# Optimization experiments

Measured on AMD Instinct MI355X. Metric: run time of the kernel, lower is better.

Reference implementation:

```python
import jax, jax.numpy as jnp
import numpy as np

D_MODEL = 1024
HIDDEN = 2816
N_EXPERTS = 8
N_ACTIVE = 2
THRESH = 1.0  # snntorch Leaky default threshold; single-step spike = (input > 1.0)


def setup_inputs() -> dict:
    key = jax.random.key(0)
    ks = jax.random.split(key, 10)
    s = 0.02
    return {
        "x": jax.random.normal(ks[0], (2, 1024, D_MODEL), jnp.float32),
        "Wg": jax.random.normal(ks[1], (D_MODEL, N_EXPERTS), jnp.float32) * s,
        "bg": jnp.zeros((N_EXPERTS,), jnp.float32),
        "W_gate": jax.random.normal(ks[2], (N_EXPERTS, D_MODEL, HIDDEN), jnp.float32) * s,
        "b_gate": jnp.zeros((N_EXPERTS, HIDDEN), jnp.float32),
        "W_up": jax.random.normal(ks[3], (N_EXPERTS, D_MODEL, HIDDEN), jnp.float32) * s,
        "b_up": jnp.zeros((N_EXPERTS, HIDDEN), jnp.float32),
        "W_down": jax.random.normal(ks[4], (N_EXPERTS, HIDDEN, D_MODEL), jnp.float32) * s,
        "b_down": jnp.zeros((N_EXPERTS, D_MODEL), jnp.float32),
    }


def reference(x, Wg, bg, W_gate, b_gate, W_up, b_up, W_down, b_down):
    B, S, D = x.shape
    xf = x.reshape(-1, D)  # [T, D]
    # spiking gate: single-step Leaky => spike = heaviside(logits - 1.0)
    gate_logits = xf @ Wg + bg  # [T, E]
    spike_out = (gate_logits > THRESH).astype(x.dtype)
    top_v, top_idx = jax.lax.top_k(spike_out, N_ACTIVE)  # [T, K]
    top_w = jax.nn.softmax(top_v, axis=-1)  # [T, K]
    # combine weights per expert: sum_k onehot(idx_k) * w_k  -> [T, E]
    combine = jnp.sum(jax.nn.one_hot(top_idx, N_EXPERTS, dtype=x.dtype) * top_w[..., None], axis=1)
    # per-expert SpikingSwiGLU: spike(gate_proj(x)) * up_proj(x) -> down_proj
    g = jnp.einsum("td,edh->teh", xf, W_gate) + b_gate  # [T, E, H]
    u = jnp.einsum("td,edh->teh", xf, W_up) + b_up
    h = (g > THRESH).astype(x.dtype) * u
    y = jnp.einsum("teh,ehd->ted", h, W_down) + b_down  # [T, E, D]
    out = jnp.einsum("ted,te->td", y, combine)
    return out.reshape(B, S, D)
```

## Files before the change

kernel.cpp:

```cpp
#include <hip/hip_runtime.h>


#define D_MODEL 1024
#define HID     2816
#define NEXP    8
#define NTOK    2048
#define NPAIR   4096
#define TM      128
#define FLAGCAP  65536
#define KC      384
#define BAND    3e-4f
#define INNER   2e-5
#define NBA     22
#define NBB     8
#define AMAX    128
#define BMAX    48

typedef short s8v __attribute__((ext_vector_type(8)));
typedef float f4v __attribute__((ext_vector_type(4)));

__device__ __forceinline__ unsigned short f2bf(float f) {
  unsigned u = __float_as_uint(f);
  u += 0x7FFFu + ((u >> 16) & 1u);
  return (unsigned short)(u >> 16);
}
__device__ __forceinline__ float bf2f(unsigned short s) {
  return __uint_as_float(((unsigned)s) << 16);
}

__device__ __forceinline__ void gld16(const unsigned short* g, unsigned short* l) {
  __builtin_amdgcn_global_load_lds(
      (const __attribute__((address_space(1))) void*)g,
      (__attribute__((address_space(3))) void*)l, 16, 0, 0);
}

__device__ __forceinline__ bool np_spike(const float* __restrict__ xr,
                                         const float* __restrict__ wcol,
                                         size_t stride, float bias) {
  float g = 0.0f;
  for (int p0 = 0; p0 < D_MODEL; p0 += KC) {
    const int pe = min(p0 + KC, D_MODEL);
    float s = 0.0f;
    for (int d = p0; d < pe; ++d)
      s = fmaf(xr[d], wcol[(size_t)d * stride], s);
    g += s;
  }
  g += bias;
  return g > 1.0f;
}

__global__ void k_convx(const float* __restrict__ x, unsigned short* __restrict__ xh,
                        unsigned short* __restrict__ xl) {
  const int i = blockIdx.x * 256 + threadIdx.x;
  const float4 v = ((const float4*)x)[i];
  ushort4 h, l;
  h.x = f2bf(v.x); l.x = f2bf(v.x - bf2f(h.x));
  h.y = f2bf(v.y); l.y = f2bf(v.y - bf2f(h.y));
  h.z = f2bf(v.z); l.z = f2bf(v.z - bf2f(h.z));
  h.w = f2bf(v.w); l.w = f2bf(v.w - bf2f(h.w));
  ((ushort4*)xh)[i] = h;
  ((ushort4*)xl)[i] = l;
}

__global__ void k_convw(const float* __restrict__ in, unsigned short* __restrict__ hi,
                        unsigned short* __restrict__ lo, int R, int C) {
  const int e = blockIdx.y;
  const int ntx = C >> 6;
  const int tx = blockIdx.x % ntx;
  const int ty = blockIdx.x / ntx;
  const float* src = in + (size_t)e * R * C;
  const size_t obase = (size_t)e * R * C;
  __shared__ float t[64][65];
  const int tid = threadIdx.x;
#pragma unroll
  for (int it = 0; it < 4; ++it) {
    const int r = it * 16 + (tid >> 4);
    const float4 v = *(const float4*)(src + (size_t)(ty * 64 + r) * C + tx * 64 + (tid & 15) * 4);
    t[r][(tid & 15) * 4 + 0] = v.x;
    t[r][(tid & 15) * 4 + 1] = v.y;
    t[r][(tid & 15) * 4 + 2] = v.z;
    t[r][(tid & 15) * 4 + 3] = v.w;
  }
  __syncthreads();
#pragma unroll
  for (int it = 0; it < 2; ++it) {
    const int c = it * 32 + (tid >> 3);
    const int d0 = (tid & 7) * 8;
    s8v vh, vl;
#pragma unroll
    for (int i = 0; i < 8; ++i) {
      const float f = t[d0 + i][c];
      const unsigned short h = f2bf(f);
      vh[i] = (short)h;
      vl[i] = (short)f2bf(f - bf2f(h));
    }
    const size_t o = obase + (size_t)(tx * 64 + c) * R + ty * 64 + d0;
    *(s8v*)(hi + o) = vh;
    if (lo) *(s8v*)(lo + o) = vl;
  }
}

__global__ void k_router(const float* __restrict__ x, const float* __restrict__ Wg,
                         const float* __restrict__ bg, int* __restrict__ top_e,
                         float* __restrict__ top_w) {
  const int t = (blockIdx.x * blockDim.x + threadIdx.x) >> 6;
  const int lane = threadIdx.x & 63;
  if (t >= NTOK) return;
  const float* xr = x + (size_t)t * D_MODEL;
  double acc[NEXP];
#pragma unroll
  for (int e = 0; e < NEXP; ++e) acc[e] = 0.0;
#pragma unroll
  for (int i = 0; i < D_MODEL / 64; ++i) {
    const int d = lane + 64 * i;
    const double xv = (double)xr[d];
    const float4 w0 = *(const float4*)(Wg + d * NEXP);
    const float4 w1 = *(const float4*)(Wg + d * NEXP + 4);
    acc[0] = fma(xv, (double)w0.x, acc[0]);
    acc[1] = fma(xv, (double)w0.y, acc[1]);
    acc[2] = fma(xv, (double)w0.z, acc[2]);
    acc[3] = fma(xv, (double)w0.w, acc[3]);
    acc[4] = fma(xv, (double)w1.x, acc[4]);
    acc[5] = fma(xv, (double)w1.y, acc[5]);
    acc[6] = fma(xv, (double)w1.z, acc[6]);
    acc[7] = fma(xv, (double)w1.w, acc[7]);
  }
#pragma unroll
  for (int e = 0; e < NEXP; ++e) {
#pragma unroll
    for (int s = 32; s > 0; s >>= 1) acc[e] += __shfl_down(acc[e], s);
  }
  if (lane == 0) {
    bool sp[NEXP];
#pragma unroll
    for (int e = 0; e < NEXP; ++e) {
      const double l = acc[e] + (double)bg[e];
      if (fabs(l - 1.0) < INNER)
        sp[e] = np_spike(xr, Wg + e, NEXP, bg[e]);
      else
        sp[e] = l > 1.0;
    }
    int e0 = -1, e1 = -1;
    for (int e = 0; e < NEXP; ++e) if (sp[e])  { if (e0 < 0) e0 = e; else if (e1 < 0) e1 = e; }
    for (int e = 0; e < NEXP; ++e) if (!sp[e]) { if (e0 < 0) e0 = e; else if (e1 < 0) e1 = e; }
    float w0v, w1v;
    if (sp[e0] == sp[e1]) { w0v = 0.5f; w1v = 0.5f; }
    else { w0v = 0.7310585786300049f; w1v = 0.2689414213699951f; }
    top_e[2 * t] = e0; top_e[2 * t + 1] = e1;
    top_w[2 * t] = w0v; top_w[2 * t + 1] = w1v;
  }
}

__global__ void k_group(const int* __restrict__ top_e,
                        int* __restrict__ pair_token, int* __restrict__ pair_expert,
                        int* __restrict__ tok_pair, int4* __restrict__ tile_tab,
                        int* __restrict__ meta,
                        int2* __restrict__ awork, int2* __restrict__ bwork) {
  __shared__ int cnt[NEXP], off[NEXP + 1], fill[NEXP];
  const int tid = threadIdx.x;
  if (tid < NEXP) { cnt[tid] = 0; fill[tid] = 0; }
  __syncthreads();
  for (int i = tid; i < NPAIR; i += 256) atomicAdd(&cnt[top_e[i]], 1);
  __syncthreads();
  if (tid == 0) {
    int tstart[NEXP], tcnt[NEXP];
    off[0] = 0;
    for (int e = 0; e < NEXP; ++e) off[e + 1] = off[e] + cnt[e];
    int nt = 0;
    for (int e = 0; e < NEXP; ++e) {
      tstart[e] = nt;
      for (int s = 0; s < cnt[e]; s += TM) {
        tile_tab[nt] = make_int4(e, off[e] + s, min(TM, cnt[e] - s), 0);
        ++nt;
      }
      tcnt[e] = nt - tstart[e];
    }
    meta[0] = nt;
    meta[1] = 0;
    for (int x = 0; x < 8; ++x) {
      int s = 0;
      for (int P = x; P < NEXP * NBA; P += 8) {
        const int e = P / NBA, bn = P % NBA;
        for (int m = 0; m < tcnt[e]; ++m)
          awork[x * AMAX + s++] = make_int2(tstart[e] + m, bn);
      }
      for (; s < AMAX; ++s) awork[x * AMAX + s] = make_int2(-1, 0);
    }
    for (int x = 0; x < 8; ++x) {
      int s = 0;
      for (int P = x; P < NEXP * NBB; P += 8) {
        const int e = P / NBB, bn = P % NBB;
        for (int m = 0; m < tcnt[e]; ++m)
          bwork[x * BMAX + s++] = make_int2(tstart[e] + m, bn);
      }
      for (; s < BMAX; ++s) bwork[x * BMAX + s] = make_int2(-1, 0);
    }
  }
  __syncthreads();
  for (int i = tid; i < NPAIR; i += 256) {
    const int e = top_e[i];
    const int pos = off[e] + atomicAdd(&fill[e], 1);
    pair_token[pos] = i >> 1;
    pair_expert[pos] = e;
    tok_pair[i] = pos;
  }
}

__launch_bounds__(256, 2)
__global__ void k_stage_a_bf(const unsigned short* __restrict__ xh,
                             const unsigned short* __restrict__ xl,
                             const unsigned short* __restrict__ wgh,
                             const unsigned short* __restrict__ wgl,
                             const unsigned short* __restrict__ wuh,
                             const float* __restrict__ bgate, const float* __restrict__ bup,
                             const int* __restrict__ pair_token,
                             const int4* __restrict__ tile_tab,
                             const int2* __restrict__ awork,
                             int* meta,
                             unsigned short* __restrict__ hbuf,
                             unsigned int* __restrict__ flags) {
  const int2 wk = awork[(blockIdx.x & 7) * AMAX + (blockIdx.x >> 3)];
  if (wk.x < 0) return;
  const int4 tt = tile_tab[wk.x];
  const int e = tt.x, row0 = tt.y, rows = tt.z;
  const int n0 = wk.y * 128;

  __shared__ __align__(16) unsigned short lds[5 * 4096];

  const int tid = threadIdx.x;
  const int lane = tid & 63;
  const int wid = tid >> 6;
  const int wmb = (wid >> 1) * 4;
  const int wnb = (wid & 1) * 4;

  const unsigned short* p[10];
#pragma unroll
  for (int c = 0; c < 10; ++c) {
    const int idx = tid + 256 * c;
    const int arr = idx >> 9;
    const int q = idx & 511;
    const int rn = ((q >> 6) << 4) + (q & 15);
    const int j = (q & 63) >> 4;
    if (arr < 2) {
      if (rn < rows) {
        const int tok = pair_token[row0 + rn];
        p[c] = (arr ? xl : xh) + (size_t)tok * D_MODEL + 8 * j;
      } else p[c] = xh;
    } else {
      const unsigned short* base = (arr == 2) ? wgh : (arr == 3) ? wgl : wuh;
      p[c] = base + ((size_t)e * HID + n0 + rn) * D_MODEL + 8 * j;
    }
  }

  const f4v fz = {0.f, 0.f, 0.f, 0.f};
  f4v acc_g[4][4], acc_u[4][4];
#pragma unroll
  for (int m = 0; m < 4; ++m)
#pragma unroll
    for (int n = 0; n < 4; ++n) { acc_g[m][n] = fz; acc_u[m][n] = fz; }

  for (int k0 = 0; k0 < D_MODEL; k0 += 32) {
#pragma unroll
    for (int c = 0; c < 10; ++c)
      gld16(p[c] + k0, lds + (((c << 8) + (tid & 192)) << 3));
    __syncthreads();
    s8v afh[4], afl[4];
#pragma unroll
    for (int m = 0; m < 4; ++m) {
      afh[m] = *(const s8v*)(lds + ((wmb + m) * 64 + lane) * 8);
      afl[m] = *(const s8v*)(lds + 4096 + ((wmb + m) * 64 + lane) * 8);
    }
#pragma unroll
    for (int n = 0; n < 4; ++n) {
      const int boff = ((wnb + n) * 64 + lane) * 8;
      const s8v bgh = *(const s8v*)(lds + 8192 + boff);
      const s8v bgl = *(const s8v*)(lds + 12288 + boff);
      const s8v buh = *(const s8v*)(lds + 16384 + boff);
#pragma unroll
      for (int m = 0; m < 4; ++m) {
        acc_g[m][n] = __builtin_amdgcn_mfma_f32_16x16x32_bf16(afh[m], bgh, acc_g[m][n], 0, 0, 0);
        acc_g[m][n] = __builtin_amdgcn_mfma_f32_16x16x32_bf16(afh[m], bgl, acc_g[m][n], 0, 0, 0);
        acc_g[m][n] = __builtin_amdgcn_mfma_f32_16x16x32_bf16(afl[m], bgh, acc_g[m][n], 0, 0, 0);
        acc_u[m][n] = __builtin_amdgcn_mfma_f32_16x16x32_bf16(afh[m], buh, acc_u[m][n], 0, 0, 0);
      }
    }
    __syncthreads();
  }

  const int lcol = lane & 15;
  const int lrow = (lane >> 4) * 4;
#pragma unroll
  for (int n = 0; n < 4; ++n) {
    const int col = n0 + (wnb + n) * 16 + lcol;
    const float bgv = bgate[e * HID + col];
    const float buv = bup[e * HID + col];
#pragma unroll
    for (int m = 0; m < 4; ++m) {
#pragma unroll
      for (int i = 0; i < 4; ++i) {
        const int r = (wmb + m) * 16 + lrow + i;
        if (r < rows) {
          const float g = acc_g[m][n][i] + bgv;
          const float u = acc_u[m][n][i] + buv;
          hbuf[(size_t)(row0 + r) * HID + col] = f2bf(g > 1.0f ? u : 0.0f);
          if (fabsf(g - 1.0f) < BAND) {
            const unsigned idx = atomicAdd((unsigned*)(meta + 1), 1u);
            if (idx < FLAGCAP) flags[idx] = ((unsigned)(row0 + r) << 16) | (unsigned)col;
          }
        }
      }
    }
  }
}

__launch_bounds__(256, 2)
__global__ void k_stage_b_bf(const unsigned short* __restrict__ hbuf,
                             const unsigned short* __restrict__ wdh,
                             const int4* __restrict__ tile_tab,
                             const int2* __restrict__ bwork,
                             float* __restrict__ ybuf) {
  const int2 wk = bwork[(blockIdx.x & 7) * BMAX + (blockIdx.x >> 3)];
  if (wk.x < 0) return;
  const int4 tt = tile_tab[wk.x];
  const int e = tt.x, row0 = tt.y, rows = tt.z;
  const int n0 = wk.y * 128;

  __shared__ __align__(16) unsigned short lds[2 * 8192];

  const int tid = threadIdx.x;
  const int lane = tid & 63;
  const int wid = tid >> 6;
  const int wmb = (wid >> 1) * 4;
  const int wnb = (wid & 1) * 4;

  const unsigned short* p[8];
#pragma unroll
  for (int c = 0; c < 8; ++c) {
    const int idx = tid + 256 * c;
    const int arr = idx >> 10;
    const int q = idx & 1023;
    const int rn = ((q >> 7) << 4) + (q & 15);
    const int j = (q & 127) >> 4;
    if (arr == 0) {
      p[c] = (rn < rows) ? (hbuf + (size_t)(row0 + rn) * HID + 8 * j) : hbuf;
    } else {
      p[c] = wdh + ((size_t)e * D_MODEL + n0 + rn) * HID + 8 * j;
    }
  }

  const f4v fz = {0.f, 0.f, 0.f, 0.f};
  f4v acc[4][4];
#pragma unroll
  for (int m = 0; m < 4; ++m)
#pragma unroll
    for (int n = 0; n < 4; ++n) acc[m][n] = fz;

  for (int k0 = 0; k0 < HID; k0 += 64) {
#pragma unroll
    for (int c = 0; c < 8; ++c)
      gld16(p[c] + k0, lds + (((c << 8) + (tid & 192)) << 3));
    __syncthreads();
#pragma unroll
    for (int kk = 0; kk < 2; ++kk) {
      s8v af[4];
#pragma unroll
      for (int m = 0; m < 4; ++m)
        af[m] = *(const s8v*)(lds + ((wmb + m) * 128 + kk * 64 + lane) * 8);
#pragma unroll
      for (int n = 0; n < 4; ++n) {
        const s8v bv = *(const s8v*)(lds + 8192 + ((wnb + n) * 128 + kk * 64 + lane) * 8);
#pragma unroll
        for (int m = 0; m < 4; ++m)
          acc[m][n] = __builtin_amdgcn_mfma_f32_16x16x32_bf16(af[m], bv, acc[m][n], 0, 0, 0);
      }
    }
    __syncthreads();
  }

  const int lcol = lane & 15;
  const int lrow = (lane >> 4) * 4;
#pragma unroll
  for (int m = 0; m < 4; ++m)
#pragma unroll
    for (int i = 0; i < 4; ++i) {
      const int r = (wmb + m) * 16 + lrow + i;
      if (r < rows) {
#pragma unroll
        for (int n = 0; n < 4; ++n) {
          const int col = n0 + (wnb + n) * 16 + lcol;
          ybuf[(size_t)(row0 + r) * D_MODEL + col] = acc[m][n][i];
        }
      }
    }
}

__global__ void k_patch(const float* __restrict__ x,
                        const float* __restrict__ Wgate, const float* __restrict__ bgate,
                        const float* __restrict__ Wup, const float* __restrict__ bup,
                        const int* __restrict__ pair_token, const int* __restrict__ pair_expert,
                        const int* __restrict__ meta, const unsigned* __restrict__ flags,
                        unsigned short* __restrict__ hbuf) {
  const int nw = (gridDim.x * blockDim.x) >> 6;
  const int w = (blockIdx.x * blockDim.x + threadIdx.x) >> 6;
  const int lane = threadIdx.x & 63;
  int n = meta[1];
  if (n > FLAGCAP) n = FLAGCAP;
  for (int f = w; f < n; f += nw) {
    const unsigned fl = flags[f];
    const int row = (int)(fl >> 16);
    const int col = (int)(fl & 0xFFFFu);
    const int tok = pair_token[row];
    const int e = pair_expert[row];
    const float* xr = x + (size_t)tok * D_MODEL;
    const float* wg = Wgate + (size_t)e * D_MODEL * HID + col;
    const float* wu = Wup + (size_t)e * D_MODEL * HID + col;
    double g = 0.0, u = 0.0;
#pragma unroll
    for (int i = 0; i < D_MODEL / 64; ++i) {
      const int d = lane + 64 * i;
      const double xv = (double)xr[d];
      g = fma(xv, (double)wg[(size_t)d * HID], g);
      u = fma(xv, (double)wu[(size_t)d * HID], u);
    }
#pragma unroll
    for (int s = 32; s > 0; s >>= 1) { g += __shfl_down(g, s); u += __shfl_down(u, s); }
    if (lane == 0) {
      g += (double)bgate[e * HID + col];
      u += (double)bup[e * HID + col];
      bool spike;
      if (fabs(g - 1.0) < INNER)
        spike = np_spike(xr, wg, HID, bgate[e * HID + col]);
      else
        spike = g > 1.0;
      hbuf[(size_t)row * HID + col] = f2bf(spike ? (float)u : 0.0f);
    }
  }
}

__global__ void k_combine(const float* __restrict__ ybuf, const float* __restrict__ bdown,
                          const int* __restrict__ tok_pair, const int* __restrict__ top_e,
                          const float* __restrict__ top_w, float* __restrict__ out) {
  const int t = blockIdx.x;
  const int c = threadIdx.x;
  const int p0 = tok_pair[2 * t], p1 = tok_pair[2 * t + 1];
  const float w0 = top_w[2 * t], w1 = top_w[2 * t + 1];
  const int e0 = top_e[2 * t], e1 = top_e[2 * t + 1];
  const float4 y0 = ((const float4*)(ybuf + (size_t)p0 * D_MODEL))[c];
  const float4 y1 = ((const float4*)(ybuf + (size_t)p1 * D_MODEL))[c];
  const float4 b0 = ((const float4*)(bdown + (size_t)e0 * D_MODEL))[c];
  const float4 b1 = ((const float4*)(bdown + (size_t)e1 * D_MODEL))[c];
  float4 o;
  o.x = w0 * (y0.x + b0.x) + w1 * (y1.x + b1.x);
  o.y = w0 * (y0.y + b0.y) + w1 * (y1.y + b1.y);
  o.z = w0 * (y0.z + b0.z) + w1 * (y1.z + b1.z);
  o.w = w0 * (y0.w + b0.w) + w1 * (y1.w + b1.w);
  ((float4*)(out + (size_t)t * D_MODEL))[c] = o;
}

extern "C" void kernel_launch(void* const* d_in, const int* in_sizes, int n_in,
                              void* d_out, int out_size, void* d_ws, size_t ws_size,
                              hipStream_t stream) {
  const float* x     = (const float*)d_in[0];
  const float* Wg    = (const float*)d_in[1];
  const float* bg    = (const float*)d_in[2];
  const float* Wgate = (const float*)d_in[3];
  const float* bgate = (const float*)d_in[4];
  const float* Wup   = (const float*)d_in[5];
  const float* bup   = (const float*)d_in[6];
  const float* Wdown = (const float*)d_in[7];
  const float* bdown = (const float*)d_in[8];
  float* out = (float*)d_out;

  char* ws = (char*)d_ws;
  unsigned short* xh   = (unsigned short*)(ws + 0);
  unsigned short* xl   = (unsigned short*)(ws + 4194304);
  unsigned short* hbuf = (unsigned short*)(ws + 8388608);
  float* ybuf          = (float*)(ws + 31457280);
  int* top_e           = (int*)(ws + 48234496);
  float* top_w         = (float*)(ws + 48250880);
  int* pair_token      = (int*)(ws + 48267264);
  int* pair_expert     = (int*)(ws + 48283648);
  int* tok_pair        = (int*)(ws + 48300032);
  int4* tile_tab       = (int4*)(ws + 48316416);
  int* meta            = (int*)(ws + 48317184);
  unsigned* flags      = (unsigned*)(ws + 48317440);
  int2* awork          = (int2*)(ws + 48579584);
  int2* bwork          = (int2*)(ws + 48587776);
  unsigned short* wgh  = (unsigned short*)(ws + 48590848);
  unsigned short* wgl  = (unsigned short*)(ws + 94728192);
  unsigned short* wuh  = (unsigned short*)(ws + 140865536);
  unsigned short* wdh  = (unsigned short*)(ws + 187002880);

  k_convx<<<dim3(NTOK * D_MODEL / 4 / 256), dim3(256), 0, stream>>>(x, xh, xl);
  k_convw<<<dim3(44 * 16, NEXP), dim3(256), 0, stream>>>(Wgate, wgh, wgl, D_MODEL, HID);
  k_convw<<<dim3(44 * 16, NEXP), dim3(256), 0, stream>>>(Wup, wuh, nullptr, D_MODEL, HID);
  k_convw<<<dim3(16 * 44, NEXP), dim3(256), 0, stream>>>(Wdown, wdh, nullptr, HID, D_MODEL);
  k_router<<<dim3(NTOK / 4), dim3(256), 0, stream>>>(x, Wg, bg, top_e, top_w);
  k_group<<<dim3(1), dim3(256), 0, stream>>>(top_e, pair_token, pair_expert, tok_pair,
                                             tile_tab, meta, awork, bwork);
  k_stage_a_bf<<<dim3(8 * AMAX), dim3(256), 0, stream>>>(
      xh, xl, wgh, wgl, wuh, bgate, bup, pair_token, tile_tab, awork, meta, hbuf, flags);
  k_patch<<<dim3(512), dim3(256), 0, stream>>>(x, Wgate, bgate, Wup, bup, pair_token,
                                               pair_expert, meta, flags, hbuf);
  k_stage_b_bf<<<dim3(8 * BMAX), dim3(256), 0, stream>>>(
      hbuf, wdh, tile_tab, bwork, ybuf);
  k_combine<<<dim3(NTOK), dim3(256), 0, stream>>>(ybuf, bdown, tok_pair, top_e, top_w, out);
}
```

Baseline: 559.4 us.

## Double-buffer LDS tiles in expert GEMMs and parallelize work-list construction

```diff
diff --git a/kernel.cpp b/kernel.cpp
--- a/kernel.cpp
+++ b/kernel.cpp
@@ -15,6 +15,8 @@
 #define NBB     8
 #define AMAX    128
 #define BMAX    48
+#define ABUF    20480
+#define BBUF    16384
 
 typedef short s8v __attribute__((ext_vector_type(8)));
 typedef float f4v __attribute__((ext_vector_type(4)));
@@ -156,14 +158,13 @@
                         int* __restrict__ tok_pair, int4* __restrict__ tile_tab,
                         int* __restrict__ meta,
                         int2* __restrict__ awork, int2* __restrict__ bwork) {
-  __shared__ int cnt[NEXP], off[NEXP + 1], fill[NEXP];
+  __shared__ int cnt[NEXP], off[NEXP + 1], fill[NEXP], tstart[NEXP], tcnt[NEXP];
   const int tid = threadIdx.x;
   if (tid < NEXP) { cnt[tid] = 0; fill[tid] = 0; }
   __syncthreads();
   for (int i = tid; i < NPAIR; i += 256) atomicAdd(&cnt[top_e[i]], 1);
   __syncthreads();
   if (tid == 0) {
-    int tstart[NEXP], tcnt[NEXP];
     off[0] = 0;
     for (int e = 0; e < NEXP; ++e) off[e + 1] = off[e] + cnt[e];
     int nt = 0;
@@ -177,26 +178,30 @@
     }
     meta[0] = nt;
     meta[1] = 0;
-    for (int x = 0; x < 8; ++x) {
-      int s = 0;
-      for (int P = x; P < NEXP * NBA; P += 8) {
-        const int e = P / NBA, bn = P % NBA;
-        for (int m = 0; m < tcnt[e]; ++m)
-          awork[x * AMAX + s++] = make_int2(tstart[e] + m, bn);
-      }
-      for (; s < AMAX; ++s) awork[x * AMAX + s] = make_int2(-1, 0);
-    }
-    for (int x = 0; x < 8; ++x) {
-      int s = 0;
-      for (int P = x; P < NEXP * NBB; P += 8) {
-        const int e = P / NBB, bn = P % NBB;
-        for (int m = 0; m < tcnt[e]; ++m)
-          bwork[x * BMAX + s++] = make_int2(tstart[e] + m, bn);
-      }
-      for (; s < BMAX; ++s) bwork[x * BMAX + s] = make_int2(-1, 0);
-    }
-  }
-  __syncthreads();
+  }
+  __syncthreads();
+  for (int i = tid; i < 8 * AMAX; i += 256) awork[i] = make_int2(-1, 0);
+  for (int i = tid; i < 8 * BMAX; i += 256) bwork[i] = make_int2(-1, 0);
+  __syncthreads();
+  if (tid < 8 * (NEXP * NBA / 8)) {
+    const int x = tid & 7, i = tid >> 3;
+    const int P = x + 8 * i;
+    const int e = P / NBA, bn = P % NBA;
+    int slot = 0;
+    for (int j = 0; j < i; ++j) slot += tcnt[(x + 8 * j) / NBA];
+    for (int m = 0; m < tcnt[e]; ++m)
+      awork[x * AMAX + slot + m] = make_int2(tstart[e] + m, bn);
+  }
+  if (tid >= 192 && tid < 192 + 8 * (NEXP * NBB / 8)) {
+    const int t2 = tid - 192;
+    const int x = t2 & 7, i = t2 >> 3;
+    const int P = x + 8 * i;
+    const int e = P / NBB, bn = P % NBB;
+    int slot = 0;
+    for (int j = 0; j < i; ++j) slot += tcnt[(x + 8 * j) / NBB];
+    for (int m = 0; m < tcnt[e]; ++m)
+      bwork[x * BMAX + slot + m] = make_int2(tstart[e] + m, bn);
+  }
   for (int i = tid; i < NPAIR; i += 256) {
     const int e = top_e[i];
     const int pos = off[e] + atomicAdd(&fill[e], 1);
@@ -225,13 +230,14 @@
   const int e = tt.x, row0 = tt.y, rows = tt.z;
   const int n0 = wk.y * 128;
 
-  __shared__ __align__(16) unsigned short lds[5 * 4096];
+  __shared__ __align__(16) unsigned short lds[2 * ABUF];
 
   const int tid = threadIdx.x;
   const int lane = tid & 63;
   const int wid = tid >> 6;
   const int wmb = (wid >> 1) * 4;
   const int wnb = (wid & 1) * 4;
+  const int sbase = ((tid & 192)) << 3;
 
   const unsigned short* p[10];
 #pragma unroll
@@ -259,23 +265,32 @@
 #pragma unroll
     for (int n = 0; n < 4; ++n) { acc_g[m][n] = fz; acc_u[m][n] = fz; }
 
+#pragma unroll
+  for (int c = 0; c < 10; ++c)
+    gld16(p[c], lds + ((c << 11) + sbase));
+  __syncthreads();
+
+  int cur = 0;
   for (int k0 = 0; k0 < D_MODEL; k0 += 32) {
-#pragma unroll
-    for (int c = 0; c < 10; ++c)
-      gld16(p[c] + k0, lds + (((c << 8) + (tid & 192)) << 3));
-    __syncthreads();
+    unsigned short* const L  = lds + (cur ? ABUF : 0);
+    if (k0 + 32 < D_MODEL) {
+      unsigned short* const Lp = lds + (cur ? 0 : ABUF);
+#pragma unroll
+      for (int c = 0; c < 10; ++c)
+        gld16(p[c] + k0 + 32, Lp + ((c << 11) + sbase));
+    }
     s8v afh[4], afl[4];
 #pragma unroll
     for (int m = 0; m < 4; ++m) {
-      afh[m] = *(const s8v*)(lds + ((wmb + m) * 64 + lane) * 8);
-      afl[m] = *(const s8v*)(lds + 4096 + ((wmb + m) * 64 + lane) * 8);
+      afh[m] = *(const s8v*)(L + ((wmb + m) * 64 + lane) * 8);
+      afl[m] = *(const s8v*)(L + 4096 + ((wmb + m) * 64 + lane) * 8);
     }
 #pragma unroll
     for (int n = 0; n < 4; ++n) {
       const int boff = ((wnb + n) * 64 + lane) * 8;
-      const s8v bgh = *(const s8v*)(lds + 8192 + boff);
-      const s8v bgl = *(const s8v*)(lds + 12288 + boff);
-      const s8v buh = *(const s8v*)(lds + 16384 + boff);
+      const s8v bgh = *(const s8v*)(L + 8192 + boff);
+      const s8v bgl = *(const s8v*)(L + 12288 + boff);
+      const s8v buh = *(const s8v*)(L + 16384 + boff);
 #pragma unroll
       for (int m = 0; m < 4; ++m) {
         acc_g[m][n] = __builtin_amdgcn_mfma_f32_16x16x32_bf16(afh[m], bgh, acc_g[m][n], 0, 0, 0);
@@ -285,6 +300,7 @@
       }
     }
     __syncthreads();
+    cur ^= 1;
   }
 
   const int lcol = lane & 15;
@@ -325,13 +341,14 @@
   const int e = tt.x, row0 = tt.y, rows = tt.z;
   const int n0 = wk.y * 128;
 
-  __shared__ __align__(16) unsigned short lds[2 * 8192];
+  __shared__ __align__(16) unsigned short lds[2 * BBUF];
 
   const int tid = threadIdx.x;
   const int lane = tid & 63;
   const int wid = tid >> 6;
   const int wmb = (wid >> 1) * 4;
   const int wnb = (wid & 1) * 4;
+  const int sbase = ((tid & 192)) << 3;
 
   const unsigned short* p[8];
 #pragma unroll
@@ -355,26 +372,36 @@
 #pragma unroll
     for (int n = 0; n < 4; ++n) acc[m][n] = fz;
 
+#pragma unroll
+  for (int c = 0; c < 8; ++c)
+    gld16(p[c], lds + ((c << 11) + sbase));
+  __syncthreads();
+
+  int cur = 0;
   for (int k0 = 0; k0 < HID; k0 += 64) {
-#pragma unroll
-    for (int c = 0; c < 8; ++c)
-      gld16(p[c] + k0, lds + (((c << 8) + (tid & 192)) << 3));
-    __syncthreads();
+    unsigned short* const L = lds + (cur ? BBUF : 0);
+    if (k0 + 64 < HID) {
+      unsigned short* const Lp = lds + (cur ? 0 : BBUF);
+#pragma unroll
+      for (int c = 0; c < 8; ++c)
+        gld16(p[c] + k0 + 64, Lp + ((c << 11) + sbase));
+    }
 #pragma unroll
     for (int kk = 0; kk < 2; ++kk) {
       s8v af[4];
 #pragma unroll
       for (int m = 0; m < 4; ++m)
-        af[m] = *(const s8v*)(lds + ((wmb + m) * 128 + kk * 64 + lane) * 8);
+        af[m] = *(const s8v*)(L + ((wmb + m) * 128 + kk * 64 + lane) * 8);
 #pragma unroll
       for (int n = 0; n < 4; ++n) {
-        const s8v bv = *(const s8v*)(lds + 8192 + ((wnb + n) * 128 + kk * 64 + lane) * 8);
+        const s8v bv = *(const s8v*)(L + 8192 + ((wnb + n) * 128 + kk * 64 + lane) * 8);
 #pragma unroll
         for (int m = 0; m < 4; ++m)
           acc[m][n] = __builtin_amdgcn_mfma_f32_16x16x32_bf16(af[m], bv, acc[m][n], 0, 0, 0);
       }
     }
     __syncthreads();
+    cur ^= 1;
   }
 
   const int lcol = lane & 15;
```

Measured after the change: 521.9 us. -6.7%, faster.

## Halve MoE GEMM row tiles, narrow stage-B tiles, parallelize work-list build

Applied to the files above, without the earlier changes.

```diff
diff --git a/kernel.cpp b/kernel.cpp
--- a/kernel.cpp
+++ b/kernel.cpp
@@ -6,15 +6,15 @@
 #define NEXP    8
 #define NTOK    2048
 #define NPAIR   4096
-#define TM      128
-#define FLAGCAP  65536
+#define TM      64
+#define FLAGCAP  32768
 #define KC      384
 #define BAND    3e-4f
 #define INNER   2e-5
 #define NBA     22
-#define NBB     8
-#define AMAX    128
-#define BMAX    48
+#define NBB     16
+#define AMAX    256
+#define BMAX    160
 
 typedef short s8v __attribute__((ext_vector_type(8)));
 typedef float f4v __attribute__((ext_vector_type(4)));
@@ -156,14 +156,13 @@
                         int* __restrict__ tok_pair, int4* __restrict__ tile_tab,
                         int* __restrict__ meta,
                         int2* __restrict__ awork, int2* __restrict__ bwork) {
-  __shared__ int cnt[NEXP], off[NEXP + 1], fill[NEXP];
+  __shared__ int cnt[NEXP], off[NEXP + 1], fill[NEXP], tstart[NEXP], tcnt[NEXP];
   const int tid = threadIdx.x;
   if (tid < NEXP) { cnt[tid] = 0; fill[tid] = 0; }
   __syncthreads();
   for (int i = tid; i < NPAIR; i += 256) atomicAdd(&cnt[top_e[i]], 1);
   __syncthreads();
   if (tid == 0) {
-    int tstart[NEXP], tcnt[NEXP];
     off[0] = 0;
     for (int e = 0; e < NEXP; ++e) off[e + 1] = off[e] + cnt[e];
     int nt = 0;
@@ -177,26 +176,29 @@
     }
     meta[0] = nt;
     meta[1] = 0;
-    for (int x = 0; x < 8; ++x) {
-      int s = 0;
-      for (int P = x; P < NEXP * NBA; P += 8) {
-        const int e = P / NBA, bn = P % NBA;
-        for (int m = 0; m < tcnt[e]; ++m)
-          awork[x * AMAX + s++] = make_int2(tstart[e] + m, bn);
-      }
-      for (; s < AMAX; ++s) awork[x * AMAX + s] = make_int2(-1, 0);
-    }
-    for (int x = 0; x < 8; ++x) {
-      int s = 0;
-      for (int P = x; P < NEXP * NBB; P += 8) {
-        const int e = P / NBB, bn = P % NBB;
-        for (int m = 0; m < tcnt[e]; ++m)
-          bwork[x * BMAX + s++] = make_int2(tstart[e] + m, bn);
-      }
-      for (; s < BMAX; ++s) bwork[x * BMAX + s] = make_int2(-1, 0);
-    }
   }
   __syncthreads();
+  for (int i = tid; i < 8 * AMAX; i += 256) awork[i] = make_int2(-1, 0);
+  for (int i = tid; i < 8 * BMAX; i += 256) bwork[i] = make_int2(-1, 0);
+  __syncthreads();
+  if (tid < 8 * NBA) {
+    const int x = tid & 7, i = tid >> 3;
+    const int P = x + 8 * i;
+    const int e = P / NBA, bn = P % NBA;
+    int slot = 0;
+    for (int j = 0; j < i; ++j) slot += tcnt[(x + 8 * j) / NBA];
+    for (int m = 0; m < tcnt[e]; ++m)
+      awork[x * AMAX + slot + m] = make_int2(tstart[e] + m, bn);
+  }
+  if (tid < 8 * NBB) {
+    const int x = tid & 7, i = tid >> 3;
+    const int P = x + 8 * i;
+    const int e = P / NBB, bn = P % NBB;
+    int slot = 0;
+    for (int j = 0; j < i; ++j) slot += tcnt[(x + 8 * j) / NBB];
+    for (int m = 0; m < tcnt[e]; ++m)
+      bwork[x * BMAX + slot + m] = make_int2(tstart[e] + m, bn);
+  }
   for (int i = tid; i < NPAIR; i += 256) {
     const int e = top_e[i];
     const int pos = off[e] + atomicAdd(&fill[e], 1);
@@ -206,7 +208,7 @@
   }
 }
 
-__launch_bounds__(256, 2)
+__launch_bounds__(256, 4)
 __global__ void k_stage_a_bf(const unsigned short* __restrict__ xh,
                              const unsigned short* __restrict__ xl,
                              const unsigned short* __restrict__ wgh,
@@ -225,63 +227,65 @@
   const int e = tt.x, row0 = tt.y, rows = tt.z;
   const int n0 = wk.y * 128;
 
-  __shared__ __align__(16) unsigned short lds[5 * 4096];
+  __shared__ __align__(16) unsigned short lds[2048 * 8];
 
   const int tid = threadIdx.x;
   const int lane = tid & 63;
   const int wid = tid >> 6;
-  const int wmb = (wid >> 1) * 4;
-  const int wnb = (wid & 1) * 4;
-
-  const unsigned short* p[10];
-#pragma unroll
-  for (int c = 0; c < 10; ++c) {
+  const int fnb = wid * 2;
+
+  const unsigned short* p[8];
+#pragma unroll
+  for (int c = 0; c < 8; ++c) {
     const int idx = tid + 256 * c;
-    const int arr = idx >> 9;
-    const int q = idx & 511;
-    const int rn = ((q >> 6) << 4) + (q & 15);
-    const int j = (q & 63) >> 4;
-    if (arr < 2) {
+    if (idx < 512) {
+      const int q = idx & 255;
+      const int rn = ((q >> 6) << 4) + (q & 15);
+      const int j = (q & 63) >> 4;
       if (rn < rows) {
         const int tok = pair_token[row0 + rn];
-        p[c] = (arr ? xl : xh) + (size_t)tok * D_MODEL + 8 * j;
+        p[c] = ((idx >> 8) ? xl : xh) + (size_t)tok * D_MODEL + 8 * j;
       } else p[c] = xh;
     } else {
-      const unsigned short* base = (arr == 2) ? wgh : (arr == 3) ? wgl : wuh;
+      const int b = (idx - 512) >> 9;
+      const int q = (idx - 512) & 511;
+      const int rn = ((q >> 6) << 4) + (q & 15);
+      const int j = (q & 63) >> 4;
+      const unsigned short* base = (b == 0) ? wgh : (b == 1) ? wgl : wuh;
       p[c] = base + ((size_t)e * HID + n0 + rn) * D_MODEL + 8 * j;
     }
   }
 
   const f4v fz = {0.f, 0.f, 0.f, 0.f};
-  f4v acc_g[4][4], acc_u[4][4];
+  f4v acc_g[4][2], acc_u[4][2];
 #pragma unroll
   for (int m = 0; m < 4; ++m)
 #pragma unroll
-    for (int n = 0; n < 4; ++n) { acc_g[m][n] = fz; acc_u[m][n] = fz; }
+    for (int n = 0; n < 2; ++n) { acc_g[m][n] = fz; acc_u[m][n] = fz; }
 
   for (int k0 = 0; k0 < D_MODEL; k0 += 32) {
 #pragma unroll
-    for (int c = 0; c < 10; ++c)
+    for (int c = 0; c < 8; ++c)
       gld16(p[c] + k0, lds + (((c << 8) + (tid & 192)) << 3));
     __syncthreads();
-    s8v afh[4], afl[4];
+    s8v bgh[2], bgl[2], buh[2];
+#pragma unroll
+    for (int n = 0; n < 2; ++n) {
+      const int boff = ((fnb + n) * 64 + lane) * 8;
+      bgh[n] = *(const s8v*)(lds + 4096 + boff);
+      bgl[n] = *(const s8v*)(lds + 8192 + boff);
+      buh[n] = *(const s8v*)(lds + 12288 + boff);
+    }
 #pragma unroll
     for (int m = 0; m < 4; ++m) {
-      afh[m] = *(const s8v*)(lds + ((wmb + m) * 64 + lane) * 8);
-      afl[m] = *(const s8v*)(lds + 4096 + ((wmb + m) * 64 + lane) * 8);
-    }
-#pragma unroll
-    for (int n = 0; n < 4; ++n) {
-      const int boff = ((wnb + n) * 64 + lane) * 8;
-      const s8v bgh = *(const s8v*)(lds + 8192 + boff);
-      const s8v bgl = *(const s8v*)(lds + 12288 + boff);
-      const s8v buh = *(const s8v*)(lds + 16384 + boff);
-#pragma unroll
-      for (int m = 0; m < 4; ++m) {
-        acc_g[m][n] = __builtin_amdgcn_mfma_f32_16x16x32_bf16(afh[m], bgh, acc_g[m][n], 0, 0, 0);
-        acc_g[m][n] = __builtin_amdgcn_mfma_f32_16x16x32_bf16(afh[m], bgl, acc_g[m][n], 0, 0, 0);
-        acc_g[m][n] = __builtin_amdgcn_mfma_f32_16x16x32_bf16(afl[m], bgh, acc_g[m][n], 0, 0, 0);
-        acc_u[m][n] = __builtin_amdgcn_mfma_f32_16x16x32_bf16(afh[m], buh, acc_u[m][n], 0, 0, 0);
+      const s8v afh = *(const s8v*)(lds + (m * 64 + lane) * 8);
+      const s8v afl = *(const s8v*)(lds + 2048 + (m * 64 + lane) * 8);
+#pragma unroll
+      for (int n = 0; n < 2; ++n) {
+        acc_g[m][n] = __builtin_amdgcn_mfma_f32_16x16x32_bf16(afh, bgh[n], acc_g[m][n], 0, 0, 0);
+        acc_g[m][n] = __builtin_amdgcn_mfma_f32_16x16x32_bf16(afh, bgl[n], acc_g[m][n], 0, 0, 0);
+        acc_g[m][n] = __builtin_amdgcn_mfma_f32_16x16x32_bf16(afl, bgh[n], acc_g[m][n], 0, 0, 0);
+        acc_u[m][n] = __builtin_amdgcn_mfma_f32_16x16x32_bf16(afh, buh[n], acc_u[m][n], 0, 0, 0);
       }
     }
     __syncthreads();
@@ -290,15 +294,15 @@
   const int lcol = lane & 15;
   const int lrow = (lane >> 4) * 4;
 #pragma unroll
-  for (int n = 0; n < 4; ++n) {
-    const int col = n0 + (wnb + n) * 16 + lcol;
+  for (int n = 0; n < 2; ++n) {
+    const int col = n0 + (fnb + n) * 16 + lcol;
     const float bgv = bgate[e * HID + col];
     const float buv = bup[e * HID + col];
 #pragma unroll
     for (int m = 0; m < 4; ++m) {
 #pragma unroll
       for (int i = 0; i < 4; ++i) {
-        const int r = (wmb + m) * 16 + lrow + i;
+        const int r = m * 16 + lrow + i;
         if (r < rows) {
           const float g = acc_g[m][n][i] + bgv;
           const float u = acc_u[m][n][i] + buv;
@@ -313,7 +317,7 @@
   }
 }
 
-__launch_bounds__(256, 2)
+__launch_bounds__(256, 4)
 __global__ void k_stage_b_bf(const unsigned short* __restrict__ hbuf,
                              const unsigned short* __restrict__ wdh,
                              const int4* __restrict__ tile_tab,
@@ -323,22 +327,20 @@
   if (wk.x < 0) return;
   const int4 tt = tile_tab[wk.x];
   const int e = tt.x, row0 = tt.y, rows = tt.z;
-  const int n0 = wk.y * 128;
-
-  __shared__ __align__(16) unsigned short lds[2 * 8192];
+  const int n0 = wk.y * 64;
+
+  __shared__ __align__(16) unsigned short lds[1024 * 8];
 
   const int tid = threadIdx.x;
   const int lane = tid & 63;
   const int wid = tid >> 6;
-  const int wmb = (wid >> 1) * 4;
-  const int wnb = (wid & 1) * 4;
-
-  const unsigned short* p[8];
-#pragma unroll
-  for (int c = 0; c < 8; ++c) {
+
+  const unsigned short* p[4];
+#pragma unroll
+  for (int c = 0; c < 4; ++c) {
     const int idx = tid + 256 * c;
-    const int arr = idx >> 10;
-    const int q = idx & 1023;
+    const int arr = idx >> 9;
+    const int q = idx & 511;
     const int rn = ((q >> 7) << 4) + (q & 15);
     const int j = (q & 127) >> 4;
     if (arr == 0) {
@@ -349,29 +351,22 @@
   }
 
   const f4v fz = {0.f, 0.f, 0.f, 0.f};
-  f4v acc[4][4];
-#pragma unroll
-  for (int m = 0; m < 4; ++m)
-#pragma unroll
-    for (int n = 0; n < 4; ++n) acc[m][n] = fz;
+  f4v acc[4];
+#pragma unroll
+  for (int m = 0; m < 4; ++m) acc[m] = fz;
 
   for (int k0 = 0; k0 < HID; k0 += 64) {
 #pragma unroll
-    for (int c = 0; c < 8; ++c)
+    for (int c = 0; c < 4; ++c)
       gld16(p[c] + k0, lds + (((c << 8) + (tid & 192)) << 3));
     __syncthreads();
 #pragma unroll
     for (int kk = 0; kk < 2; ++kk) {
-      s8v af[4];
-#pragma unroll
-      for (int m = 0; m < 4; ++m)
-        af[m] = *(const s8v*)(lds + ((wmb + m) * 128 + kk * 64 + lane) * 8);
-#pragma unroll
-      for (int n = 0; n < 4; ++n) {
-        const s8v bv = *(const s8v*)(lds + 8192 + ((wnb + n) * 128 + kk * 64 + lane) * 8);
-#pragma unroll
-        for (int m = 0; m < 4; ++m)
-          acc[m][n] = __builtin_amdgcn_mfma_f32_16x16x32_bf16(af[m], bv, acc[m][n], 0, 0, 0);
+      const s8v bv = *(const s8v*)(lds + 4096 + (wid * 128 + kk * 64 + lane) * 8);
+#pragma unroll
+      for (int m = 0; m < 4; ++m) {
+        const s8v af = *(const s8v*)(lds + (m * 128 + kk * 64 + lane) * 8);
+        acc[m] = __builtin_amdgcn_mfma_f32_16x16x32_bf16(af, bv, acc[m], 0, 0, 0);
       }
     }
     __syncthreads();
@@ -379,18 +374,14 @@
 
   const int lcol = lane & 15;
   const int lrow = (lane >> 4) * 4;
+  const int col = n0 + wid * 16 + lcol;
 #pragma unroll
   for (int m = 0; m < 4; ++m)
 #pragma unroll
     for (int i = 0; i < 4; ++i) {
-      const int r = (wmb + m) * 16 + lrow + i;
-      if (r < rows) {
-#pragma unroll
-        for (int n = 0; n < 4; ++n) {
-          const int col = n0 + (wnb + n) * 16 + lcol;
-          ybuf[(size_t)(row0 + r) * D_MODEL + col] = acc[m][n][i];
-        }
-      }
+      const int r = m * 16 + lrow + i;
+      if (r < rows)
+        ybuf[(size_t)(row0 + r) * D_MODEL + col] = acc[m][i];
     }
 }
 
@@ -482,22 +473,22 @@
   int* pair_expert     = (int*)(ws + 48283648);
   int* tok_pair        = (int*)(ws + 48300032);
   int4* tile_tab       = (int4*)(ws + 48316416);
-  int* meta            = (int*)(ws + 48317184);
-  unsigned* flags      = (unsigned*)(ws + 48317440);
-  int2* awork          = (int2*)(ws + 48579584);
-  int2* bwork          = (int2*)(ws + 48587776);
+  int* meta            = (int*)(ws + 48318464);
+  unsigned* flags      = (unsigned*)(ws + 48318592);
+  int2* awork          = (int2*)(ws + 48449664);
+  int2* bwork          = (int2*)(ws + 48466048);
   unsigned short* wgh  = (unsigned short*)(ws + 48590848);
   unsigned short* wgl  = (unsigned short*)(ws + 94728192);
   unsigned short* wuh  = (unsigned short*)(ws + 140865536);
   unsigned short* wdh  = (unsigned short*)(ws + 187002880);
 
   k_convx<<<dim3(NTOK * D_MODEL / 4 / 256), dim3(256), 0, stream>>>(x, xh, xl);
-  k_convw<<<dim3(44 * 16, NEXP), dim3(256), 0, stream>>>(Wgate, wgh, wgl, D_MODEL, HID);
-  k_convw<<<dim3(44 * 16, NEXP), dim3(256), 0, stream>>>(Wup, wuh, nullptr, D_MODEL, HID);
-  k_convw<<<dim3(16 * 44, NEXP), dim3(256), 0, stream>>>(Wdown, wdh, nullptr, HID, D_MODEL);
   k_router<<<dim3(NTOK / 4), dim3(256), 0, stream>>>(x, Wg, bg, top_e, top_w);
   k_group<<<dim3(1), dim3(256), 0, stream>>>(top_e, pair_token, pair_expert, tok_pair,
                                              tile_tab, meta, awork, bwork);
+  k_convw<<<dim3(16 * 44, NEXP), dim3(256), 0, stream>>>(Wdown, wdh, nullptr, HID, D_MODEL);
+  k_convw<<<dim3(44 * 16, NEXP), dim3(256), 0, stream>>>(Wup, wuh, nullptr, D_MODEL, HID);
+  k_convw<<<dim3(44 * 16, NEXP), dim3(256), 0, stream>>>(Wgate, wgh, wgl, D_MODEL, HID);
   k_stage_a_bf<<<dim3(8 * AMAX), dim3(256), 0, stream>>>(
       xh, xl, wgh, wgl, wuh, bgate, bup, pair_token, tile_tab, awork, meta, hbuf, flags);
   k_patch<<<dim3(512), dim3(256), 0, stream>>>(x, Wgate, bgate, Wup, bup, pair_token,
```

Result: slower. 584.0 us (+4.4%).
